# Optimization experiments

Measured on AMD Instinct MI355X. Metric: run time of the kernel, lower is better.

The kernel has to match this reference:

```python
import jax, jax.numpy as jnp
import numpy as np

DIM = 768
NUM_HEADS = 12
HEAD_DIM = DIM // NUM_HEADS
SCALE = HEAD_DIM ** -0.5


def setup_inputs() -> dict:
    key = jax.random.key(0)
    k_x, k_m, k_qkv, k_proj, k_b = jax.random.split(key, 5)
    B, N, C = 4, 2048, DIM
    x = jax.random.normal(k_x, (B, N, C), dtype=jnp.float32)
    # boolean mask [N, N]; True = masked position (masked_fill semantics)
    mask = jax.random.randint(k_m, (N, N), 0, 2).astype(jnp.bool_)
    # qkv Linear(dim, 3*dim, bias=False): store as [C, 3C] for x @ W
    w_qkv = jax.random.normal(k_qkv, (C, 3 * C), dtype=jnp.float32) * (C ** -0.5)
    # proj Linear(dim, dim) with bias
    w_proj = jax.random.normal(k_proj, (C, C), dtype=jnp.float32) * (C ** -0.5)
    b_proj = jax.random.normal(k_b, (C,), dtype=jnp.float32) * 0.02
    return {"x": x, "mask": mask, "w_qkv": w_qkv, "w_proj": w_proj, "b_proj": b_proj}


def reference(x, mask, w_qkv, w_proj, b_proj):
    B, N, C = x.shape
    H, D = NUM_HEADS, HEAD_DIM
    qkv = (x @ w_qkv).reshape(B, N, 3, H, D)
    q = qkv[:, :, 0].transpose(0, 2, 1, 3)  # [B, H, N, D]
    k = qkv[:, :, 1].transpose(0, 2, 1, 3)
    v = qkv[:, :, 2].transpose(0, 2, 1, 3)
    attn = jnp.einsum("bhnd,bhmd->bhnm", q, k) * SCALE  # [B, H, N, N]
    attn = jnp.where(mask[None, None, :, :], -jnp.inf, attn)
    attn = jax.nn.softmax(attn, axis=-1)
    # dropout p=0.0 (eval) -> identity
    out = jnp.einsum("bhnm,bhmd->bhnd", attn, v)  # [B, H, N, D]
    out = out.transpose(0, 2, 1, 3).reshape(B, N, C)
    return out @ w_proj + b_proj
```

## Files before the change

kernel.cpp:

```cpp
#include <hip/hip_runtime.h>

#define NSEQ 2048
#define CDIM 768
#define NBATCH 4
#define NHEAD 12
#define HD 64
#define MTOT (NBATCH * NSEQ)
#define NQKV (3 * CDIM)

typedef float f32x4 __attribute__((ext_vector_type(4)));
typedef short bf16x8 __attribute__((ext_vector_type(8)));
typedef short short4v __attribute__((ext_vector_type(4)));

__device__ __forceinline__ short f2bf(float f) {
  union { float f; unsigned u; } x; x.f = f;
  unsigned r = x.u + 0x7fffu + ((x.u >> 16) & 1u);
  return (short)(r >> 16);
}

__device__ __forceinline__ float exp2a(float x) {
  float r; asm("v_exp_f32 %0, %1" : "=v"(r) : "v"(x)); return r;
}

__device__ __forceinline__ void gload16(const short* g, short* l) {
  __builtin_amdgcn_global_load_lds((const __attribute__((address_space(1))) void*)g,
                                   (__attribute__((address_space(3))) void*)l, 16, 0, 0);
}

__device__ __forceinline__ const bf16x8* frag(const short* t, int row, int col) {
  int byt = (row << 7) + (col << 1);
  byt ^= (row & 7) << 4;
  return (const bf16x8*)((const char*)t + byt);
}

__global__ __launch_bounds__(256) void detect_mask(const unsigned char* __restrict__ m,
                                                   int* __restrict__ flag) {
  __shared__ int f1, f23;
  if (threadIdx.x == 0) { f1 = 0; f23 = 0; }
  __syncthreads();
  int a = 0, b = 0;
  for (int i = threadIdx.x; i < 1024; i += 256) {
    if (m[i * 4 + 1]) a = 1;
    if (m[i * 4 + 2] | m[i * 4 + 3]) b = 1;
  }
  if (a) atomicOr(&f1, 1);
  if (b) atomicOr(&f23, 1);
  __syncthreads();
  if (threadIdx.x == 0) *flag = f1 ? 1 : (f23 ? 2 : 0);
}

__global__ __launch_bounds__(256) void pack_mask(const void* __restrict__ mask,
                                                 const int* __restrict__ flag,
                                                 unsigned* __restrict__ bits) {
  int wi = blockIdx.x * 256 + threadIdx.x;
  int f = *flag;
  unsigned v = 0;
  if (f == 1) {
    const unsigned char* p = (const unsigned char*)mask + (size_t)wi * 32;
#pragma unroll
    for (int j = 0; j < 32; ++j) v |= (p[j] != 0 ? 1u : 0u) << j;
  } else if (f == 2) {
    const float* p = (const float*)mask + (size_t)wi * 32;
#pragma unroll
    for (int j = 0; j < 32; ++j) v |= (p[j] != 0.f ? 1u : 0u) << j;
  } else {
    const int* p = (const int*)mask + (size_t)wi * 32;
#pragma unroll
    for (int j = 0; j < 32; ++j) v |= (p[j] != 0 ? 1u : 0u) << j;
  }
  bits[wi] = v;
}

__global__ __launch_bounds__(256) void conv_bf16(const float* __restrict__ in,
                                                 short* __restrict__ out, int n) {
  int i = (blockIdx.x * 256 + threadIdx.x) * 8;
  if (i >= n) return;
  f32x4 a = *(const f32x4*)&in[i];
  f32x4 b = *(const f32x4*)&in[i + 4];
  bf16x8 o;
#pragma unroll
  for (int j = 0; j < 4; ++j) o[j] = f2bf(a[j]);
#pragma unroll
  for (int j = 0; j < 4; ++j) o[4 + j] = f2bf(b[j]);
  *(bf16x8*)&out[i] = o;
}

__global__ __launch_bounds__(256) void transpose_conv(const float* __restrict__ in,
                                                      short* __restrict__ outp,
                                                      int R, int Cc) {
  __shared__ short tile[64][65];
  int c0 = blockIdx.x * 64, r0 = blockIdx.y * 64;
  int t = threadIdx.x;
  int tr = t >> 4;
  int tc = (t & 15) * 4;
  for (int rr = tr; rr < 64; rr += 16) {
    f32x4 v = *(const f32x4*)&in[(size_t)(r0 + rr) * Cc + c0 + tc];
#pragma unroll
    for (int j = 0; j < 4; ++j) tile[tc + j][rr] = f2bf(v[j]);
  }
  __syncthreads();
  for (int cc = tr; cc < 64; cc += 16) {
#pragma unroll
    for (int j = 0; j < 4; ++j)
      outp[(size_t)(c0 + cc) * R + r0 + tc + j] = tile[cc][tc + j];
  }
}

__global__ __launch_bounds__(256) void vtrans(const short* __restrict__ qkvb,
                                              short* __restrict__ vt) {
  __shared__ short t[64][72];
  int n0 = blockIdx.x * 64, bh = blockIdx.y;
  int b = bh / NHEAD, h = bh % NHEAD;
  int tid = threadIdx.x, r = tid >> 2, c0 = (tid & 3) * 16;
  const short* src = qkvb + (size_t)(b * NSEQ + n0 + r) * NQKV + 2 * CDIM + h * HD + c0;
  bf16x8 v0 = *(const bf16x8*)src;
  bf16x8 v1 = *(const bf16x8*)(src + 8);
  *(bf16x8*)&t[r][c0] = v0;
  *(bf16x8*)&t[r][c0 + 8] = v1;
  __syncthreads();
  bf16x8 o0, o1;
#pragma unroll
  for (int j = 0; j < 8; ++j) { o0[j] = t[c0 + j][r]; o1[j] = t[c0 + 8 + j][r]; }
  short* dst = vt + (size_t)(bh * HD + r) * NSEQ + n0 + c0;
  *(bf16x8*)&dst[0] = o0;
  *(bf16x8*)&dst[8] = o1;
}

template <bool F32OUT>
__global__ __launch_bounds__(256) void gemm_bt(const short* __restrict__ A,
                                               const short* __restrict__ Bt,
                                               void* __restrict__ Cout,
                                               const float* __restrict__ bias,
                                               int Mdim, int Ndim, int Kdim) {
  __shared__ short As[2][128 * 32];
  __shared__ short Bs[2][128 * 32];
  const int tid = threadIdx.x;
  const int lane = tid & 63;
  const int w = tid >> 6;
  const int wm = (w >> 1) * 64, wn = (w & 1) * 64;
  const int lr = lane & 15, lh = lane >> 4;
  const int m0 = blockIdx.y * 128, n0 = blockIdx.x * 128;

  f32x4 acc[4][4];
#pragma unroll
  for (int i = 0; i < 4; ++i)
#pragma unroll
    for (int j = 0; j < 4; ++j) acc[i][j] = (f32x4){0.f, 0.f, 0.f, 0.f};

  const int srow = w * 32 + (lane >> 2);
  const int scol = (lane & 3) * 8;
  const short* Ap = A + (size_t)(m0 + srow) * Kdim + scol;
  const short* Bp = Bt + (size_t)(n0 + srow) * Kdim + scol;
  const int l0 = (w * 32) * 32;
  const int l1 = (w * 32 + 16) * 32;

  auto tilecompute = [&](const short* Asb, const short* Bsb) {
    bf16x8 a[4], b[4];
#pragma unroll
    for (int i = 0; i < 4; ++i) a[i] = *(const bf16x8*)&Asb[(wm + i * 16 + lr) * 32 + lh * 8];
#pragma unroll
    for (int j = 0; j < 4; ++j) b[j] = *(const bf16x8*)&Bsb[(wn + j * 16 + lr) * 32 + lh * 8];
#pragma unroll
    for (int i = 0; i < 4; ++i)
#pragma unroll
      for (int j = 0; j < 4; ++j)
        acc[i][j] = __builtin_amdgcn_mfma_f32_16x16x32_bf16(a[i], b[j], acc[i][j], 0, 0, 0);
  };

  gload16(Ap, &As[0][l0]);
  gload16(Ap + (size_t)16 * Kdim, &As[0][l1]);
  gload16(Bp, &Bs[0][l0]);
  gload16(Bp + (size_t)16 * Kdim, &Bs[0][l1]);

  const int NT = Kdim >> 5;
  for (int t = 0; t < NT - 1; ++t) {
    const int cur = t & 1, nxt = cur ^ 1;
    const int k1 = (t + 1) << 5;
    gload16(Ap + k1, &As[nxt][l0]);
    gload16(Ap + (size_t)16 * Kdim + k1, &As[nxt][l1]);
    gload16(Bp + k1, &Bs[nxt][l0]);
    gload16(Bp + (size_t)16 * Kdim + k1, &Bs[nxt][l1]);
    asm volatile("s_waitcnt vmcnt(4)" ::: "memory");
    __builtin_amdgcn_s_barrier();
    tilecompute(As[cur], Bs[cur]);
    __builtin_amdgcn_s_barrier();
  }
  asm volatile("s_waitcnt vmcnt(0)" ::: "memory");
  __builtin_amdgcn_s_barrier();
  tilecompute(As[(NT - 1) & 1], Bs[(NT - 1) & 1]);

#pragma unroll
  for (int i = 0; i < 4; ++i) {
    int mrowb = m0 + wm + i * 16 + lh * 4;
#pragma unroll
    for (int j = 0; j < 4; ++j) {
      int ncol = n0 + wn + j * 16 + lr;
#pragma unroll
      for (int r = 0; r < 4; ++r) {
        float v = acc[i][j][r];
        if (F32OUT)
          ((float*)Cout)[(size_t)(mrowb + r) * Ndim + ncol] = v + bias[ncol];
        else
          ((short*)Cout)[(size_t)(mrowb + r) * Ndim + ncol] = f2bf(v);
      }
    }
  }
}

__global__ __launch_bounds__(256) void flash_attn(const short* __restrict__ qkv,
                                                  const short* __restrict__ vtb,
                                                  const unsigned long long* __restrict__ mbits,
                                                  short* __restrict__ outp) {
  __shared__ short KB[2][64 * 64];
  __shared__ short VB[2][64 * 64];

  const int tid = threadIdx.x;
  const int lane = tid & 63;
  const int w = tid >> 6;
  const int lr = lane & 15, lh = lane >> 4;
  const int q0 = blockIdx.x * 64;
  const int bh = blockIdx.y;
  const int b = bh / NHEAD, h = bh % NHEAD;

  const int srow = lane >> 3;
  const int schunk = (lane & 7) ^ srow;

  const short* qrow = qkv + (size_t)(b * NSEQ + q0 + w * 16 + lr) * NQKV + h * HD;
  const bf16x8 qf0 = *(const bf16x8*)(qrow + lh * 8);
  const bf16x8 qf1 = *(const bf16x8*)(qrow + 32 + lh * 8);
  asm volatile("" ::: "memory");

  const short* kbase = qkv + (size_t)(b * NSEQ + w * 16 + srow) * NQKV + CDIM + h * HD + schunk * 8;
  const short* vbase = vtb + (size_t)(bh * HD + w * 16 + srow) * NSEQ + schunk * 8;

  gload16(kbase, &KB[0][(w * 16) * 64]);
  gload16(kbase + (size_t)8 * NQKV, &KB[0][(w * 16 + 8) * 64]);
  gload16(vbase, &VB[0][(w * 16) * 64]);
  gload16(vbase + (size_t)8 * NSEQ, &VB[0][(w * 16 + 8) * 64]);

  const unsigned long long* mrow = mbits + (size_t)(q0 + w * 16 + lr) * (NSEQ / 64);
  unsigned long long mw = mrow[0];

  float m_r = -1e30f, l_r = 0.f;
  f32x4 o[4];
#pragma unroll
  for (int nd = 0; nd < 4; ++nd) o[nd] = (f32x4){0.f, 0.f, 0.f, 0.f};

  const int srcA = (lh & 1) * 32 + lr;
  const int srcB = srcA + 16;
  const int nbh = lh >> 1;
  const float C2 = 0.18033688f;

  auto compute = [&](const short* Kb, const short* Vb, unsigned long long mwv) {
    float p[4][4];
#pragma unroll
    for (int nb = 0; nb < 4; ++nb) {
      f32x4 st = (f32x4){0.f, 0.f, 0.f, 0.f};
      st = __builtin_amdgcn_mfma_f32_16x16x32_bf16(*frag(Kb, nb * 16 + lr, lh * 8), qf0, st, 0, 0, 0);
      st = __builtin_amdgcn_mfma_f32_16x16x32_bf16(*frag(Kb, nb * 16 + lr, 32 + lh * 8), qf1, st, 0, 0, 0);
      unsigned m4 = ((unsigned)(mwv >> (nb * 16 + lh * 4))) & 15u;
#pragma unroll
      for (int r = 0; r < 4; ++r)
        p[nb][r] = ((m4 >> r) & 1u) ? -3e38f : st[r] * C2;
    }

    float pm = p[0][0];
#pragma unroll
    for (int nb = 0; nb < 4; ++nb)
#pragma unroll
      for (int r = 0; r < 4; ++r) pm = fmaxf(pm, p[nb][r]);
    pm = fmaxf(pm, __shfl_xor(pm, 16, 64));
    pm = fmaxf(pm, __shfl_xor(pm, 32, 64));

    if (__any(pm > m_r + 8.f)) {
      float nm = fmaxf(m_r, pm);
      float al = exp2a(m_r - nm);
      m_r = nm;
      l_r *= al;
#pragma unroll
      for (int nd = 0; nd < 4; ++nd)
#pragma unroll
        for (int r = 0; r < 4; ++r) o[nd][r] *= al;
    }
    float rs = 0.f;
#pragma unroll
    for (int nb = 0; nb < 4; ++nb)
#pragma unroll
      for (int r = 0; r < 4; ++r) {
        float e = exp2a(p[nb][r] - m_r);
        p[nb][r] = e;
        rs += e;
      }
    rs += __shfl_xor(rs, 16, 64);
    rs += __shfl_xor(rs, 32, 64);
    l_r += rs;

    unsigned pk[4][2];
#pragma unroll
    for (int nb = 0; nb < 4; ++nb) {
      asm("v_cvt_pk_bf16_f32 %0, %1, %2" : "=v"(pk[nb][0]) : "v"(p[nb][0]), "v"(p[nb][1]));
      asm("v_cvt_pk_bf16_f32 %0, %1, %2" : "=v"(pk[nb][1]) : "v"(p[nb][2]), "v"(p[nb][3]));
    }
    bf16x8 pb[2];
#pragma unroll
    for (int c = 0; c < 2; ++c) {
      unsigned a0 = __shfl(pk[2 * c][0], srcA, 64);
      unsigned a1 = __shfl(pk[2 * c][1], srcA, 64);
      unsigned a2 = __shfl(pk[2 * c][0], srcB, 64);
      unsigned a3 = __shfl(pk[2 * c][1], srcB, 64);
      unsigned b0 = __shfl(pk[2 * c + 1][0], srcA, 64);
      unsigned b1 = __shfl(pk[2 * c + 1][1], srcA, 64);
      unsigned b2 = __shfl(pk[2 * c + 1][0], srcB, 64);
      unsigned b3 = __shfl(pk[2 * c + 1][1], srcB, 64);
      union { unsigned u[4]; bf16x8 v; } uu;
      uu.u[0] = nbh ? b0 : a0;
      uu.u[1] = nbh ? b1 : a1;
      uu.u[2] = nbh ? b2 : a2;
      uu.u[3] = nbh ? b3 : a3;
      pb[c] = uu.v;
    }

#pragma unroll
    for (int nd = 0; nd < 4; ++nd) {
      o[nd] = __builtin_amdgcn_mfma_f32_16x16x32_bf16(*frag(Vb, nd * 16 + lr, lh * 8), pb[0], o[nd], 0, 0, 0);
      o[nd] = __builtin_amdgcn_mfma_f32_16x16x32_bf16(*frag(Vb, nd * 16 + lr, 32 + lh * 8), pb[1], o[nd], 0, 0, 0);
    }
  };

  for (int t = 0; t < 31; ++t) {
    const int cur = t & 1, nxt = cur ^ 1;
    {
      const short* kb = kbase + (size_t)(t + 1) * 64 * NQKV;
      gload16(kb, &KB[nxt][(w * 16) * 64]);
      gload16(kb + (size_t)8 * NQKV, &KB[nxt][(w * 16 + 8) * 64]);
      const short* vb = vbase + (t + 1) * 64;
      gload16(vb, &VB[nxt][(w * 16) * 64]);
      gload16(vb + (size_t)8 * NSEQ, &VB[nxt][(w * 16 + 8) * 64]);
    }
    asm volatile("s_waitcnt vmcnt(4)" ::: "memory");
    unsigned long long mw_next = mrow[t + 1];
    __builtin_amdgcn_s_barrier();
    compute(KB[cur], VB[cur], mw);
    mw = mw_next;
    __builtin_amdgcn_s_barrier();
  }
  asm volatile("s_waitcnt vmcnt(0)" ::: "memory");
  __builtin_amdgcn_s_barrier();
  compute(KB[1], VB[1], mw);

  const float inv = 1.f / l_r;
  short* orow = outp + (size_t)(b * NSEQ + q0 + w * 16 + lr) * CDIM + h * HD + lh * 4;
#pragma unroll
  for (int nd = 0; nd < 4; ++nd) {
    short4v sv;
#pragma unroll
    for (int r = 0; r < 4; ++r) sv[r] = f2bf(o[nd][r] * inv);
    *(short4v*)&orow[nd * 16] = sv;
  }
}

extern "C" void kernel_launch(void* const* d_in, const int* in_sizes, int n_in,
                              void* d_out, int out_size, void* d_ws, size_t ws_size,
                              hipStream_t stream) {
  const float* x      = (const float*)d_in[0];
  const void*  mask   = d_in[1];
  const float* w_qkv  = (const float*)d_in[2];
  const float* w_proj = (const float*)d_in[3];
  const float* b_proj = (const float*)d_in[4];
  float* outp = (float*)d_out;
  char* ws = (char*)d_ws;

  int*      flag   = (int*)(ws + 0);
  unsigned* mbits  = (unsigned*)(ws + 1024);
  short*    xb     = (short*)(ws + 525312);
  short*    wqkvT  = (short*)(ws + 25691136);
  short*    wprojT = (short*)(ws + 29230080);
  short*    qkvb   = (short*)(ws + 30409728);
  short*    attnb  = (short*)(ws + 68158464);
  short*    vtb    = xb;

  detect_mask<<<1, 256, 0, stream>>>((const unsigned char*)mask, flag);
  pack_mask<<<512, 256, 0, stream>>>(mask, flag, mbits);
  conv_bf16<<<(MTOT * CDIM) / 2048, 256, 0, stream>>>(x, xb, MTOT * CDIM);
  transpose_conv<<<dim3(NQKV / 64, CDIM / 64), 256, 0, stream>>>(w_qkv, wqkvT, CDIM, NQKV);
  transpose_conv<<<dim3(CDIM / 64, CDIM / 64), 256, 0, stream>>>(w_proj, wprojT, CDIM, CDIM);
  gemm_bt<false><<<dim3(NQKV / 128, MTOT / 128), 256, 0, stream>>>(xb, wqkvT, qkvb, nullptr,
                                                                   MTOT, NQKV, CDIM);
  vtrans<<<dim3(NSEQ / 64, NBATCH * NHEAD), 256, 0, stream>>>(qkvb, vtb);
  flash_attn<<<dim3(NSEQ / 64, NBATCH * NHEAD), 256, 0, stream>>>(
      qkvb, vtb, (const unsigned long long*)mbits, attnb);
  gemm_bt<true><<<dim3(CDIM / 128, MTOT / 128), 256, 0, stream>>>(attnb, wprojT, outp, b_proj,
                                                                  MTOT, CDIM, CDIM);
}
```

Measured before the change: 308.9 us.

## Switch flash attention to 32x32 MFMA tiles with 128-query blocks

New measurement: 292.3 us. 5.4% less time.

```diff
diff --git a/kernel.cpp b/kernel.cpp
--- a/kernel.cpp
+++ b/kernel.cpp
@@ -9,6 +9,7 @@
 #define NQKV (3 * CDIM)
 
 typedef float f32x4 __attribute__((ext_vector_type(4)));
+typedef float f32x16 __attribute__((ext_vector_type(16)));
 typedef short bf16x8 __attribute__((ext_vector_type(8)));
 typedef short short4v __attribute__((ext_vector_type(4)));
 
@@ -20,6 +21,10 @@
 
 __device__ __forceinline__ float exp2a(float x) {
   float r; asm("v_exp_f32 %0, %1" : "=v"(r) : "v"(x)); return r;
+}
+
+__device__ __forceinline__ unsigned cvtpk(float lo, float hi) {
+  unsigned r; asm("v_cvt_pk_bf16_f32 %0, %1, %2" : "=v"(r) : "v"(lo), "v"(hi)); return r;
 }
 
 __device__ __forceinline__ void gload16(const short* g, short* l) {
@@ -217,17 +222,30 @@
   const int tid = threadIdx.x;
   const int lane = tid & 63;
   const int w = tid >> 6;
-  const int lr = lane & 15, lh = lane >> 4;
-  const int q0 = blockIdx.x * 64;
+  const int q5 = lane & 31, hi = lane >> 5;
+  const int q0 = blockIdx.x * 128;
   const int bh = blockIdx.y;
   const int b = bh / NHEAD, h = bh % NHEAD;
+  const int qglob = q0 + w * 32 + q5;
 
   const int srow = lane >> 3;
   const int schunk = (lane & 7) ^ srow;
 
-  const short* qrow = qkv + (size_t)(b * NSEQ + q0 + w * 16 + lr) * NQKV + h * HD;
-  const bf16x8 qf0 = *(const bf16x8*)(qrow + lh * 8);
-  const bf16x8 qf1 = *(const bf16x8*)(qrow + 32 + lh * 8);
+  const float C2 = 0.18033688f;
+  bf16x8 qf[4];
+  {
+    const short* qrow = qkv + (size_t)(b * NSEQ + qglob) * NQKV + h * HD;
+#pragma unroll
+    for (int ks = 0; ks < 4; ++ks) {
+      bf16x8 v = *(const bf16x8*)(qrow + ks * 16 + hi * 8);
+#pragma unroll
+      for (int j = 0; j < 8; ++j) {
+        union { unsigned u; float f; } c; c.u = ((unsigned)(unsigned short)v[j]) << 16;
+        v[j] = f2bf(c.f * C2);
+      }
+      qf[ks] = v;
+    }
+  }
   asm volatile("" ::: "memory");
 
   const short* kbase = qkv + (size_t)(b * NSEQ + w * 16 + srow) * NQKV + CDIM + h * HD + schunk * 8;
@@ -238,38 +256,45 @@
   gload16(vbase, &VB[0][(w * 16) * 64]);
   gload16(vbase + (size_t)8 * NSEQ, &VB[0][(w * 16 + 8) * 64]);
 
-  const unsigned long long* mrow = mbits + (size_t)(q0 + w * 16 + lr) * (NSEQ / 64);
+  const unsigned long long* mrow = mbits + (size_t)qglob * (NSEQ / 64);
   unsigned long long mw = mrow[0];
 
   float m_r = -1e30f, l_r = 0.f;
-  f32x4 o[4];
-#pragma unroll
-  for (int nd = 0; nd < 4; ++nd) o[nd] = (f32x4){0.f, 0.f, 0.f, 0.f};
-
-  const int srcA = (lh & 1) * 32 + lr;
-  const int srcB = srcA + 16;
-  const int nbh = lh >> 1;
-  const float C2 = 0.18033688f;
+  f32x16 o[2];
+#pragma unroll
+  for (int dt = 0; dt < 2; ++dt)
+#pragma unroll
+    for (int r = 0; r < 16; ++r) o[dt][r] = 0.f;
 
   auto compute = [&](const short* Kb, const short* Vb, unsigned long long mwv) {
-    float p[4][4];
-#pragma unroll
-    for (int nb = 0; nb < 4; ++nb) {
-      f32x4 st = (f32x4){0.f, 0.f, 0.f, 0.f};
-      st = __builtin_amdgcn_mfma_f32_16x16x32_bf16(*frag(Kb, nb * 16 + lr, lh * 8), qf0, st, 0, 0, 0);
-      st = __builtin_amdgcn_mfma_f32_16x16x32_bf16(*frag(Kb, nb * 16 + lr, 32 + lh * 8), qf1, st, 0, 0, 0);
-      unsigned m4 = ((unsigned)(mwv >> (nb * 16 + lh * 4))) & 15u;
-#pragma unroll
-      for (int r = 0; r < 4; ++r)
-        p[nb][r] = ((m4 >> r) & 1u) ? -3e38f : st[r] * C2;
-    }
-
-    float pm = p[0][0];
-#pragma unroll
-    for (int nb = 0; nb < 4; ++nb)
-#pragma unroll
-      for (int r = 0; r < 4; ++r) pm = fmaxf(pm, p[nb][r]);
-    pm = fmaxf(pm, __shfl_xor(pm, 16, 64));
+    f32x16 st[2];
+#pragma unroll
+    for (int kvt = 0; kvt < 2; ++kvt) {
+      f32x16 z;
+#pragma unroll
+      for (int r = 0; r < 16; ++r) z[r] = 0.f;
+#pragma unroll
+      for (int ks = 0; ks < 4; ++ks)
+        z = __builtin_amdgcn_mfma_f32_32x32x16_bf16(
+            *frag(Kb, kvt * 32 + q5, ks * 16 + hi * 8), qf[ks], z, 0, 0, 0);
+      st[kvt] = z;
+    }
+
+    unsigned msk0 = ((unsigned)mwv) >> (hi * 4);
+    unsigned msk1 = ((unsigned)(mwv >> 32)) >> (hi * 4);
+    float pm = -3e38f;
+#pragma unroll
+    for (int kvt = 0; kvt < 2; ++kvt) {
+      unsigned mk = kvt ? msk1 : msk0;
+#pragma unroll
+      for (int r = 0; r < 16; ++r) {
+        const int pos = (r & 3) + 8 * (r >> 2);
+        float sv = st[kvt][r];
+        sv = ((mk >> pos) & 1u) ? -3e38f : sv;
+        st[kvt][r] = sv;
+        pm = fmaxf(pm, sv);
+      }
+    }
     pm = fmaxf(pm, __shfl_xor(pm, 32, 64));
 
     if (__any(pm > m_r + 8.f)) {
@@ -278,53 +303,53 @@
       m_r = nm;
       l_r *= al;
 #pragma unroll
-      for (int nd = 0; nd < 4; ++nd)
-#pragma unroll
-        for (int r = 0; r < 4; ++r) o[nd][r] *= al;
-    }
-    float rs = 0.f;
-#pragma unroll
-    for (int nb = 0; nb < 4; ++nb)
-#pragma unroll
-      for (int r = 0; r < 4; ++r) {
-        float e = exp2a(p[nb][r] - m_r);
-        p[nb][r] = e;
-        rs += e;
-      }
-    rs += __shfl_xor(rs, 16, 64);
+      for (int dt = 0; dt < 2; ++dt)
+#pragma unroll
+        for (int r = 0; r < 16; ++r) o[dt][r] *= al;
+    }
+
+    float rs0 = 0.f, rs1 = 0.f;
+#pragma unroll
+    for (int r = 0; r < 16; ++r) {
+      float e0 = exp2a(st[0][r] - m_r);
+      float e1 = exp2a(st[1][r] - m_r);
+      st[0][r] = e0; st[1][r] = e1;
+      rs0 += e0; rs1 += e1;
+    }
+    float rs = rs0 + rs1;
     rs += __shfl_xor(rs, 32, 64);
     l_r += rs;
 
-    unsigned pk[4][2];
-#pragma unroll
-    for (int nb = 0; nb < 4; ++nb) {
-      asm("v_cvt_pk_bf16_f32 %0, %1, %2" : "=v"(pk[nb][0]) : "v"(p[nb][0]), "v"(p[nb][1]));
-      asm("v_cvt_pk_bf16_f32 %0, %1, %2" : "=v"(pk[nb][1]) : "v"(p[nb][2]), "v"(p[nb][3]));
-    }
-    bf16x8 pb[2];
-#pragma unroll
-    for (int c = 0; c < 2; ++c) {
-      unsigned a0 = __shfl(pk[2 * c][0], srcA, 64);
-      unsigned a1 = __shfl(pk[2 * c][1], srcA, 64);
-      unsigned a2 = __shfl(pk[2 * c][0], srcB, 64);
-      unsigned a3 = __shfl(pk[2 * c][1], srcB, 64);
-      unsigned b0 = __shfl(pk[2 * c + 1][0], srcA, 64);
-      unsigned b1 = __shfl(pk[2 * c + 1][1], srcA, 64);
-      unsigned b2 = __shfl(pk[2 * c + 1][0], srcB, 64);
-      unsigned b3 = __shfl(pk[2 * c + 1][1], srcB, 64);
-      union { unsigned u[4]; bf16x8 v; } uu;
-      uu.u[0] = nbh ? b0 : a0;
-      uu.u[1] = nbh ? b1 : a1;
-      uu.u[2] = nbh ? b2 : a2;
-      uu.u[3] = nbh ? b3 : a3;
-      pb[c] = uu.v;
-    }
-
-#pragma unroll
-    for (int nd = 0; nd < 4; ++nd) {
-      o[nd] = __builtin_amdgcn_mfma_f32_16x16x32_bf16(*frag(Vb, nd * 16 + lr, lh * 8), pb[0], o[nd], 0, 0, 0);
-      o[nd] = __builtin_amdgcn_mfma_f32_16x16x32_bf16(*frag(Vb, nd * 16 + lr, 32 + lh * 8), pb[1], o[nd], 0, 0, 0);
-    }
+    unsigned pbw[4][4];
+#pragma unroll
+    for (int ks = 0; ks < 4; ++ks) {
+      const int kvt = ks >> 1;
+      const int Ra = (ks & 1) * 8;
+      const int Rb = Ra + 4;
+      unsigned wa0 = cvtpk(st[kvt][Ra],     st[kvt][Ra + 1]);
+      unsigned wa1 = cvtpk(st[kvt][Ra + 2], st[kvt][Ra + 3]);
+      unsigned wb0 = cvtpk(st[kvt][Rb],     st[kvt][Rb + 1]);
+      unsigned wb1 = cvtpk(st[kvt][Rb + 2], st[kvt][Rb + 3]);
+      unsigned s0 = hi ? wa0 : wb0;
+      unsigned s1 = hi ? wa1 : wb1;
+      unsigned r0 = __shfl_xor(s0, 32, 64);
+      unsigned r1 = __shfl_xor(s1, 32, 64);
+      pbw[ks][0] = hi ? r0 : wa0;
+      pbw[ks][1] = hi ? r1 : wa1;
+      pbw[ks][2] = hi ? wb0 : r0;
+      pbw[ks][3] = hi ? wb1 : r1;
+    }
+
+#pragma unroll
+    for (int dt = 0; dt < 2; ++dt)
+#pragma unroll
+      for (int ks = 0; ks < 4; ++ks) {
+        union { unsigned u[4]; bf16x8 v; } pu;
+        pu.u[0] = pbw[ks][0]; pu.u[1] = pbw[ks][1];
+        pu.u[2] = pbw[ks][2]; pu.u[3] = pbw[ks][3];
+        o[dt] = __builtin_amdgcn_mfma_f32_32x32x16_bf16(
+            *frag(Vb, dt * 32 + q5, ks * 16 + hi * 8), pu.v, o[dt], 0, 0, 0);
+      }
   };
 
   for (int t = 0; t < 31; ++t) {
@@ -349,14 +374,16 @@
   compute(KB[1], VB[1], mw);
 
   const float inv = 1.f / l_r;
-  short* orow = outp + (size_t)(b * NSEQ + q0 + w * 16 + lr) * CDIM + h * HD + lh * 4;
-#pragma unroll
-  for (int nd = 0; nd < 4; ++nd) {
-    short4v sv;
-#pragma unroll
-    for (int r = 0; r < 4; ++r) sv[r] = f2bf(o[nd][r] * inv);
-    *(short4v*)&orow[nd * 16] = sv;
-  }
+  short* orow = outp + (size_t)(b * NSEQ + qglob) * CDIM + h * HD;
+#pragma unroll
+  for (int dt = 0; dt < 2; ++dt)
+#pragma unroll
+    for (int g = 0; g < 4; ++g) {
+      short4v sv;
+#pragma unroll
+      for (int r = 0; r < 4; ++r) sv[r] = f2bf(o[dt][g * 4 + r] * inv);
+      *(short4v*)&orow[dt * 32 + g * 8 + hi * 4] = sv;
+    }
 }
 
 extern "C" void kernel_launch(void* const* d_in, const int* in_sizes, int n_in,
@@ -387,7 +414,7 @@
   gemm_bt<false><<<dim3(NQKV / 128, MTOT / 128), 256, 0, stream>>>(xb, wqkvT, qkvb, nullptr,
                                                                    MTOT, NQKV, CDIM);
   vtrans<<<dim3(NSEQ / 64, NBATCH * NHEAD), 256, 0, stream>>>(qkvb, vtb);
-  flash_attn<<<dim3(NSEQ / 64, NBATCH * NHEAD), 256, 0, stream>>>(
+  flash_attn<<<dim3(NSEQ / 128, NBATCH * NHEAD), 256, 0, stream>>>(
       qkvb, vtb, (const unsigned long long*)mbits, attnb);
   gemm_bt<true><<<dim3(CDIM / 128, MTOT / 128), 256, 0, stream>>>(attnb, wprojT, outp, b_proj,
                                                                   MTOT, CDIM, CDIM);
```
